# Performance work log

Hardware: AMD Instinct MI355X
Metric: run time of the kernel (lower is better)

The kernel has to match this reference:

```python
import jax, jax.numpy as jnp
import numpy as np

N = 100000          # num_nodes
E = 1600000         # num_edges (avg degree 16)
FEAT = 16           # z-embedding dim
IN_DIM = FEAT + 4   # + 4 physics scalars
HID = 128           # hidden_dim
NUM_LAYERS = 2
NUM_REL = 3
NUM_TYPES = 4
LN_EPS = 1e-5


def setup_inputs() -> dict:
    key = jax.random.key(0)
    ks = jax.random.split(key, 20)
    s = 0.05
    return {
        "z": jax.random.randint(ks[0], (N,), 0, 100),
        "sd": jax.random.normal(ks[1], (N, 1), jnp.float32),
        "df": jax.random.normal(ks[2], (N, 1), jnp.float32),
        "cond": jax.random.normal(ks[3], (N, 1), jnp.float32),
        "mult": jax.random.normal(ks[4], (N, 1), jnp.float32),
        "node_type": jax.random.randint(ks[5], (N,), 0, NUM_TYPES),
        "edge_index": jax.random.randint(ks[6], (2, E), 0, N),
        "edge_type": jax.random.randint(ks[7], (E,), 0, NUM_REL),
        # parameters
        "z_embed": jax.random.normal(ks[8], (100, FEAT), jnp.float32) * s,
        "enc_W1": jax.random.normal(ks[9], (NUM_TYPES, IN_DIM, HID), jnp.float32) * s,
        "enc_b1": jnp.zeros((NUM_TYPES, HID), jnp.float32),
        "enc_W2": jax.random.normal(ks[10], (NUM_TYPES, HID, HID), jnp.float32) * s,
        "enc_b2": jnp.zeros((NUM_TYPES, HID), jnp.float32),
        "lin_W": jax.random.normal(ks[11], (NUM_LAYERS, HID, HID), jnp.float32) * s,
        "lin_b": jnp.zeros((NUM_LAYERS, HID), jnp.float32),
        "rel_W": jax.random.normal(ks[12], (NUM_LAYERS, NUM_REL, HID, HID), jnp.float32) * s,
        "ln_g": jnp.ones((NUM_LAYERS, HID), jnp.float32),
        "ln_b": jnp.zeros((NUM_LAYERS, HID), jnp.float32),
        "reg_W": jax.random.normal(ks[13], (HID, 1), jnp.float32) * s,
        "reg_b": jnp.zeros((1,), jnp.float32),
    }


def reference(z, sd, df, cond, mult, node_type, edge_index, edge_type,
              z_embed, enc_W1, enc_b1, enc_W2, enc_b2,
              lin_W, lin_b, rel_W, ln_g, ln_b, reg_W, reg_b):
    # FeatureBuilder: [z embedding | 4 physics scalars] -> [N, IN_DIM]
    raw = jnp.concatenate([z_embed[z], sd, df, cond, mult], axis=1)
    n = raw.shape[0]

    # TypeSpecificEncoder: per-node-type 2-layer MLP, selected by node_type
    x = jnp.zeros((n, enc_W2.shape[-1]), raw.dtype)
    for t in range(enc_W1.shape[0]):
        h = jax.nn.relu(raw @ enc_W1[t] + enc_b1[t]) @ enc_W2[t] + enc_b2[t]
        x = jnp.where((node_type == t)[:, None], h, x)

    src, dst = edge_index[0], edge_index[1]
    # degree over ALL edges (as in the torch code), clamped to >= 1
    deg = jax.ops.segment_sum(jnp.ones(src.shape[0], x.dtype), dst, num_segments=n)
    deg = jnp.clip(deg, 1.0)[:, None]

    # stacked MultiRelationGNNLayer: gather -> per-relation matmul -> scatter-add
    for l in range(lin_W.shape[0]):
        xs = x[src]                               # [E, HID] gather
        msg = jnp.zeros_like(xs)
        for r in range(rel_W.shape[1]):
            mask_r = (edge_type == r)[:, None].astype(x.dtype)
            msg = msg + (xs @ rel_W[l, r]) * mask_r
        agg = jax.ops.segment_sum(msg, dst, num_segments=n) / deg
        h = x @ lin_W[l] + lin_b[l] + agg
        # LayerNorm
        mu = jnp.mean(h, axis=-1, keepdims=True)
        var = jnp.mean((h - mu) ** 2, axis=-1, keepdims=True)
        x = (h - mu) / jnp.sqrt(var + LN_EPS) * ln_g[l] + ln_b[l]

    pooled = jnp.mean(x, axis=0)                  # [HID]
    return pooled @ reg_W + reg_b                 # [1]
```

## Files before the change

### kernel.cpp

```cpp
#include <hip/hip_runtime.h>

#define NN 100000
#define NE 1600000
#define HD 128
#define IND 20
#define LNEPS 1e-5f
#define NLIST2 400000
#define NBKT 3125
#define PASSA_B 256
#define EDGES_PER_B 6250
#define FILL_B 256
#define WCAT_B 512
#define WCATE_B 256
#define W1P_B 128
#define FILLN_B 400
#define ENC_B 12500
#define ASTRIDE 260
#define SORT_CAP 4096
#define PAD_PER_BKT 672
#define NEP (NE + NBKT * PAD_PER_BKT)
#define H1S 136
#define AES 72

typedef unsigned int uint32;
typedef unsigned short ushort16;
typedef __attribute__((ext_vector_type(8))) short bf16x8;
typedef __attribute__((ext_vector_type(4))) float f32x4;
typedef __attribute__((ext_vector_type(2))) float f32x2;

__device__ __forceinline__ ushort16 f2bf(float f) {
    uint32 u = __float_as_uint(f);
    u += 0x7fffu + ((u >> 16) & 1u);
    return (ushort16)(u >> 16);
}
__device__ __forceinline__ float bf2f1(ushort16 h) {
    return __uint_as_float(((uint32)h) << 16);
}
__device__ __forceinline__ uint32 pack2bf(float2 v) {
    return (uint32)f2bf(v.x) | ((uint32)f2bf(v.y) << 16);
}


__global__ __launch_bounds__(256) void k_hist(const int* __restrict__ ei,
                                              const int* __restrict__ et,
                                              int* __restrict__ H,
                                              ushort16* __restrict__ key16,
                                              unsigned* __restrict__ hdr32,
                                              const float* __restrict__ W2,
                                              ushort16* __restrict__ Weh,
                                              ushort16* __restrict__ Wel,
                                              const float* __restrict__ W1,
                                              ushort16* __restrict__ W1e,
                                              const int* __restrict__ nt,
                                              int* misc, unsigned* nodelist,
                                              uint32* x0, uint32* x1) {
    __shared__ int hist[NBKT];
    __shared__ int cnt4[4][4];
    __shared__ int base4[4];
    int bid = blockIdx.x, tid = threadIdx.x;

    if (bid >= PASSA_B + WCATE_B + W1P_B) {
        int rb = bid - PASSA_B - WCATE_B - W1P_B;
        int lane = tid & 63;
        int w = tid >> 6;
        if (rb == 0 && tid < 32) {
            x0[(size_t)NN * 32 + tid] = 0;
            x1[(size_t)NN * 32 + tid] = 0;
        }
        int i = rb * 256 + tid;
        int t = (i < NN) ? nt[i] : -1;
        unsigned long long lt = ((unsigned long long)1 << lane) - 1;
        int pre[4], wc[4];
#pragma unroll
        for (int tt = 0; tt < 4; tt++) {
            unsigned long long m = __ballot(t == tt);
            pre[tt] = (int)__popcll(m & lt);
            wc[tt] = (int)__popcll(m);
        }
        if (lane == 0) {
            cnt4[w][0] = wc[0]; cnt4[w][1] = wc[1];
            cnt4[w][2] = wc[2]; cnt4[w][3] = wc[3];
        }
        __syncthreads();
        if (tid < 4) {
            int tot = cnt4[0][tid] + cnt4[1][tid] + cnt4[2][tid] + cnt4[3][tid];
            base4[tid] = tot ? atomicAdd(&misc[8 + tid], tot) : 0;
        }
        __syncthreads();
        if (t >= 0) {
            int off = base4[t] + pre[t];
#pragma unroll
            for (int wp = 0; wp < 3; wp++) if (wp < w) off += cnt4[wp][t];
            nodelist[t * NN + off] = (unsigned)i | ((unsigned)t << 17);
        }
        return;
    }
    if (bid >= PASSA_B + WCATE_B) {
        int idx = (bid - PASSA_B - WCATE_B) * 256 + tid;
        int jj = idx & 7;
        int lane = (idx >> 3) & 63;
        int ntile = (idx >> 9) & 7;
        int kstep = (idx >> 12) & 1;
        int t = (idx >> 13) & 3;
        int ke = kstep * 32 + ((lane >> 4) * 8) + jj;
        int n = ntile * 16 + (lane & 15);
        float w = 0.f;
        int sel = 0;
        if (ke < 60) {
            int k0 = ke / 3;
            sel = ke - 3 * k0;
            w = W1[((size_t)t * IND + k0) * HD + n];
        }
        ushort16 hi = f2bf(w);
        W1e[idx] = (sel == 2) ? f2bf(w - bf2f1(hi)) : hi;
        return;
    }
    if (bid >= PASSA_B) {
        int idx = (bid - PASSA_B) * 256 + tid;
        int jj = idx & 7;
        int lane = (idx >> 3) & 63;
        int ntile = (idx >> 9) & 7;
        int kt = (idx >> 12) & 3;
        int t = (idx >> 14) & 3;
        int k = kt * 32 + ((lane >> 4) * 8) + jj;
        int n = ntile * 16 + (lane & 15);
        float v = W2[((size_t)t * HD + k) * HD + n];
        ushort16 hi = f2bf(v);
        Weh[idx] = hi;
        Wel[idx] = f2bf(v - bf2f1(hi));
        return;
    }

    for (int k = tid; k < NBKT; k += 256) hist[k] = 0;
    __syncthreads();
    int e0 = bid * EDGES_PER_B, e1 = e0 + EDGES_PER_B;
    for (int e = e0 + tid; e < e1; e += 256) {
        int d = ei[NE + e];
        int s = ei[e];
        int r = et[e];
        int bkt = d >> 5;
        key16[e] = (ushort16)bkt;
        hdr32[e] = (unsigned)s | ((unsigned)r << 17) | ((unsigned)(d & 31) << 19);
        atomicAdd(&hist[bkt], 1);
    }
    __syncthreads();
    for (int k = tid; k < NBKT; k += 256) H[bid * NBKT + k] = hist[k];
}


__global__ __launch_bounds__(256) void k_s1(int* __restrict__ H, int* __restrict__ btot) {
    int bkt = blockIdx.x * 256 + threadIdx.x;
    if (bkt >= NBKT) return;
    int run = 0;
    for (int jm = 0; jm < PASSA_B; jm += 8) {
        int t0 = H[(jm + 0) * NBKT + bkt];
        int t1 = H[(jm + 1) * NBKT + bkt];
        int t2 = H[(jm + 2) * NBKT + bkt];
        int t3 = H[(jm + 3) * NBKT + bkt];
        int t4 = H[(jm + 4) * NBKT + bkt];
        int t5 = H[(jm + 5) * NBKT + bkt];
        int t6 = H[(jm + 6) * NBKT + bkt];
        int t7 = H[(jm + 7) * NBKT + bkt];
        H[(jm + 0) * NBKT + bkt] = run; run += t0;
        H[(jm + 1) * NBKT + bkt] = run; run += t1;
        H[(jm + 2) * NBKT + bkt] = run; run += t2;
        H[(jm + 3) * NBKT + bkt] = run; run += t3;
        H[(jm + 4) * NBKT + bkt] = run; run += t4;
        H[(jm + 5) * NBKT + bkt] = run; run += t5;
        H[(jm + 6) * NBKT + bkt] = run; run += t6;
        H[(jm + 7) * NBKT + bkt] = run; run += t7;
    }
    btot[bkt] = run;
}

__global__ __launch_bounds__(1024) void k_s2(const int* __restrict__ btot,
                                             int* __restrict__ boff) {
    __shared__ int s[1024];
    int t = threadIdx.x;
    int v4[4];
    int sum = 0;
#pragma unroll
    for (int i = 0; i < 4; i++) {
        int idx = t * 4 + i;
        v4[i] = (idx < NBKT) ? btot[idx] : 0;
        sum += v4[i];
    }
    s[t] = sum;
    __syncthreads();
    for (int o = 1; o < 1024; o <<= 1) {
        int tv = (t >= o) ? s[t - o] : 0;
        __syncthreads();
        s[t] += tv;
        __syncthreads();
    }
    int run = s[t] - sum;
#pragma unroll
    for (int i = 0; i < 4; i++) {
        int idx = t * 4 + i;
        if (idx < NBKT) boff[idx] = run;
        run += v4[i];
    }
    if (t == 1023) boff[NBKT] = NE;
}


__global__ __launch_bounds__(256) void k_fill2(
        const ushort16* __restrict__ key16, const unsigned* __restrict__ hdr32,
        const int* __restrict__ H, const int* __restrict__ boff,
        unsigned* __restrict__ packed,
        const unsigned* __restrict__ nodelist, const int* __restrict__ z,
        const float* __restrict__ sd, const float* __restrict__ df,
        const float* __restrict__ cond, const float* __restrict__ mult,
        const float* __restrict__ z_embed,
        const ushort16* __restrict__ W1e, const float* __restrict__ b1,
        const float* __restrict__ b2,
        unsigned char* __restrict__ xout,
        const float* __restrict__ rel_W, const float* __restrict__ lin_W,
        ushort16* __restrict__ Wbh, ushort16* __restrict__ Wbl,
        const ushort16* __restrict__ Weh, const ushort16* __restrict__ Wel) {
    __shared__ __attribute__((aligned(16))) char smem[13440];
    int bid = blockIdx.x;
    int tid = threadIdx.x;

    if (bid < FILL_B) {
        int* cur = (int*)smem;
        for (int k = tid; k < NBKT; k += 256)
            cur[k] = boff[k] + H[bid * NBKT + k];
        __syncthreads();
        int e0 = bid * EDGES_PER_B, e1 = e0 + EDGES_PER_B;
        for (int e = e0 + tid; e < e1; e += 256) {
            int kb = (int)key16[e];
            int p = atomicAdd(&cur[kb], 1);
            packed[p] = hdr32[e];
        }
        return;
    }
    int j = bid - FILL_B;
    if (j < WCAT_B) {
        int idx = j * 256 + tid;
        int jj = idx & 7;
        int lane = (idx >> 3) & 63;
        int ntile = (idx >> 9) & 7;
        int kt = (idx >> 12) & 15;
        int l = (idx >> 16) & 1;
        int k = kt * 32 + ((lane >> 4) * 8) + jj;
        int n = ntile * 16 + (lane & 15);
        float v;
        if (k < 384) v = rel_W[((l * 3 + (k >> 7)) * HD + (k & 127)) * HD + n];
        else         v = lin_W[(l * HD + (k - 384)) * HD + n];
        ushort16 hi = f2bf(v);
        Wbh[idx] = hi;
        Wbl[idx] = f2bf(v - bf2f1(hi));
        return;
    }
    j -= WCAT_B;
    if (j >= ENC_B) return;

    ushort16* Ae  = (ushort16*)smem;
    ushort16* h1b = (ushort16*)(smem + 4608);
    unsigned* ent = (unsigned*)(smem + 4608 + 8704);

    int base = j * 32;
    if (tid < 32) ent[tid] = nodelist[base + tid];
    if (tid >= 64 && tid < 128) {
        int r = (tid - 64) >> 1, c = 30 + (tid & 1);
        ((uint32*)Ae)[r * 36 + c] = 0;
    }
    __syncthreads();
    if (ent[0] == 0xFFFFFFFFu) return;
    int type = (int)(ent[0] >> 17);

    for (int idx = tid; idx < 32 * 20; idx += 256) {
        int nl = idx / 20, f = idx - nl * 20;
        unsigned e = ent[nl];
        float v = 0.f;
        if (e != 0xFFFFFFFFu) {
            int node = (int)(e & 0x1FFFF);
            if (f < 16)      v = z_embed[z[node] * 16 + f];
            else if (f == 16) v = sd[node];
            else if (f == 17) v = df[node];
            else if (f == 18) v = cond[node];
            else              v = mult[node];
        }
        ushort16 hi = f2bf(v);
        ushort16 lo = f2bf(v - bf2f1(hi));
        ushort16* ap = Ae + nl * AES + 3 * f;
        ap[0] = hi; ap[1] = lo; ap[2] = hi;
    }
    __syncthreads();

    int lane = tid & 63, wv = tid >> 6;
    int nt0 = 2 * wv, nt1 = 2 * wv + 1;
    int mrow0 = lane & 15, mrow1 = 16 + (lane & 15);
    int koff = (lane >> 4) * 8;

    {
        f32x4 e00 = {0.f, 0.f, 0.f, 0.f}, e01 = e00, e10 = e00, e11 = e00;
        const bf16x8* w1p = (const bf16x8*)(W1e + (size_t)type * 8192);
#pragma unroll
        for (int ks = 0; ks < 2; ks++) {
            bf16x8 af0 = *(const bf16x8*)&Ae[mrow0 * AES + ks * 32 + koff];
            bf16x8 af1 = *(const bf16x8*)&Ae[mrow1 * AES + ks * 32 + koff];
            bf16x8 bf0 = w1p[(ks * 8 + nt0) * 64 + lane];
            bf16x8 bf1 = w1p[(ks * 8 + nt1) * 64 + lane];
            e00 = __builtin_amdgcn_mfma_f32_16x16x32_bf16(af0, bf0, e00, 0, 0, 0);
            e01 = __builtin_amdgcn_mfma_f32_16x16x32_bf16(af0, bf1, e01, 0, 0, 0);
            e10 = __builtin_amdgcn_mfma_f32_16x16x32_bf16(af1, bf0, e10, 0, 0, 0);
            e11 = __builtin_amdgcn_mfma_f32_16x16x32_bf16(af1, bf1, e11, 0, 0, 0);
        }
        int c0 = nt0 * 16 + (lane & 15), c1 = nt1 * 16 + (lane & 15);
        float bb0 = b1[type * HD + c0], bb1 = b1[type * HD + c1];
        int rb2 = (lane >> 4) * 4;
#pragma unroll
        for (int r = 0; r < 4; r++) {
            h1b[(rb2 + r) * H1S + c0]      = f2bf(fmaxf(e00[r] + bb0, 0.f));
            h1b[(rb2 + r) * H1S + c1]      = f2bf(fmaxf(e01[r] + bb1, 0.f));
            h1b[(16 + rb2 + r) * H1S + c0] = f2bf(fmaxf(e10[r] + bb0, 0.f));
            h1b[(16 + rb2 + r) * H1S + c1] = f2bf(fmaxf(e11[r] + bb1, 0.f));
        }
    }
    __syncthreads();

    f32x4 a00 = {0.f, 0.f, 0.f, 0.f}, a01 = a00, a10 = a00, a11 = a00;
    const bf16x8* weh = (const bf16x8*)(Weh + (size_t)type * 16384);
    const bf16x8* wel = (const bf16x8*)(Wel + (size_t)type * 16384);
    const ushort16* h1p = h1b;
#pragma unroll
    for (int kt = 0; kt < 4; kt++) {
        bf16x8 af0 = *(const bf16x8*)&h1p[mrow0 * H1S + kt * 32 + koff];
        bf16x8 af1 = *(const bf16x8*)&h1p[mrow1 * H1S + kt * 32 + koff];
        bf16x8 bh0 = weh[(kt * 8 + nt0) * 64 + lane];
        bf16x8 bh1 = weh[(kt * 8 + nt1) * 64 + lane];
        bf16x8 bl0 = wel[(kt * 8 + nt0) * 64 + lane];
        bf16x8 bl1 = wel[(kt * 8 + nt1) * 64 + lane];
        a00 = __builtin_amdgcn_mfma_f32_16x16x32_bf16(af0, bh0, a00, 0, 0, 0);
        a01 = __builtin_amdgcn_mfma_f32_16x16x32_bf16(af0, bh1, a01, 0, 0, 0);
        a10 = __builtin_amdgcn_mfma_f32_16x16x32_bf16(af1, bh0, a10, 0, 0, 0);
        a11 = __builtin_amdgcn_mfma_f32_16x16x32_bf16(af1, bh1, a11, 0, 0, 0);
        a00 = __builtin_amdgcn_mfma_f32_16x16x32_bf16(af0, bl0, a00, 0, 0, 0);
        a01 = __builtin_amdgcn_mfma_f32_16x16x32_bf16(af0, bl1, a01, 0, 0, 0);
        a10 = __builtin_amdgcn_mfma_f32_16x16x32_bf16(af1, bl0, a10, 0, 0, 0);
        a11 = __builtin_amdgcn_mfma_f32_16x16x32_bf16(af1, bl1, a11, 0, 0, 0);
    }
    int c0 = nt0 * 16 + (lane & 15), c1 = nt1 * 16 + (lane & 15);
    float b20 = b2[type * HD + c0], b21 = b2[type * HD + c1];
    int rb = (lane >> 4) * 4;
#pragma unroll
    for (int r = 0; r < 4; r++) {
        int r0 = rb + r, r1 = 16 + rb + r;
        unsigned e0v = ent[r0], e1v = ent[r1];
        if (e0v != 0xFFFFFFFFu) {
            int node = (int)(e0v & 0x1FFFF);
            int p0 = __builtin_amdgcn_cvt_pk_fp8_f32(a00[r] + b20, a00[r] + b20, 0, false);
            int p1 = __builtin_amdgcn_cvt_pk_fp8_f32(a01[r] + b21, a01[r] + b21, 0, false);
            xout[(size_t)node * HD + c0] = (unsigned char)(p0 & 0xff);
            xout[(size_t)node * HD + c1] = (unsigned char)(p1 & 0xff);
        }
        if (e1v != 0xFFFFFFFFu) {
            int node = (int)(e1v & 0x1FFFF);
            int p0 = __builtin_amdgcn_cvt_pk_fp8_f32(a10[r] + b20, a10[r] + b20, 0, false);
            int p1 = __builtin_amdgcn_cvt_pk_fp8_f32(a11[r] + b21, a11[r] + b21, 0, false);
            xout[(size_t)node * HD + c0] = (unsigned char)(p0 & 0xff);
            xout[(size_t)node * HD + c1] = (unsigned char)(p1 & 0xff);
        }
    }
}


__global__ __launch_bounds__(256) void k_sort2(const unsigned* __restrict__ packed,
                                               const int* __restrict__ boff,
                                               unsigned* __restrict__ packed2,
                                               int* __restrict__ off,
                                               int* __restrict__ degarr) {
    __shared__ unsigned ebuf[SORT_CAP];
    __shared__ int hs[96];
    __shared__ int cur[96];
    __shared__ int segp[97];
    __shared__ int scn[128];
    int b = blockIdx.x;
    int tid = threadIdx.x;
    int base = boff[b];
    int tot = boff[b + 1] - base;
    if (tot > SORT_CAP) tot = SORT_CAP;
    int pb = base + PAD_PER_BKT * b;

    if (tid < 96) hs[tid] = 0;
    for (int e = tid; e < tot; e += 256) ebuf[e] = packed[base + e];
    __syncthreads();
    for (int e = tid; e < tot; e += 256) {
        unsigned h = ebuf[e];
        int key = (int)(h >> 19) * 3 + (int)((h >> 17) & 3);
        atomicAdd(&hs[key], 1);
    }
    __syncthreads();
    int padv = (tid < 96) ? ((hs[tid] + 7) & ~7) : 0;
    if (tid < 128) scn[tid] = padv;
    __syncthreads();
#pragma unroll
    for (int o = 1; o < 128; o <<= 1) {
        int tv = (tid < 128 && tid >= o) ? scn[tid - o] : 0;
        __syncthreads();
        if (tid < 128) scn[tid] += tv;
        __syncthreads();
    }
    if (tid < 96) segp[tid] = scn[tid] - padv;
    if (tid == 95) segp[96] = scn[95];
    __syncthreads();
    if (tid < 96) {
        cur[tid] = segp[tid];
        off[((b * 32 + tid / 3) << 2) + (tid % 3)] = pb + segp[tid];
    }
    if (tid >= 96 && tid < 128) {
        int n = tid - 96;
        off[((b * 32 + n) << 2) + 3] = pb + segp[3 * n + 3];
        degarr[b * 32 + n] = hs[3 * n] + hs[3 * n + 1] + hs[3 * n + 2];
    }
    __syncthreads();
    for (int e = tid; e < tot; e += 256) {
        unsigned h = ebuf[e];
        int key = (int)(h >> 19) * 3 + (int)((h >> 17) & 3);
        int p = atomicAdd(&cur[key], 1);
        packed2[pb + p] = h & 0x1FFFF;
    }
    __syncthreads();
    if (tid < 96) {
        int e0 = segp[tid] + hs[tid];
        int e1 = segp[tid + 1];
        for (int q = e0; q < e1; q++) packed2[pb + q] = NN;
    }
}


#define LOADU8(U, Q)                                                          \
    U##0 = x[(int)Q##0 * 64 + lane]; U##1 = x[(int)Q##1 * 64 + lane];         \
    U##2 = x[(int)Q##2 * 64 + lane]; U##3 = x[(int)Q##3 * 64 + lane];         \
    U##4 = x[(int)Q##4 * 64 + lane]; U##5 = x[(int)Q##5 * 64 + lane];         \
    U##6 = x[(int)Q##6 * 64 + lane]; U##7 = x[(int)Q##7 * 64 + lane];

#define LOADQ8(Q, E)                                                          \
    Q##0 = packed[(E)];     Q##1 = packed[(E) + 1];                           \
    Q##2 = packed[(E) + 2]; Q##3 = packed[(E) + 3];                           \
    Q##4 = packed[(E) + 4]; Q##5 = packed[(E) + 5];                           \
    Q##6 = packed[(E) + 6]; Q##7 = packed[(E) + 7];

#define SUM8(S, U) {                                                          \
    f32x2 v0 = __builtin_amdgcn_cvt_pk_f32_fp8(U##0, false);                  \
    f32x2 v1 = __builtin_amdgcn_cvt_pk_f32_fp8(U##1, false);                  \
    f32x2 v2 = __builtin_amdgcn_cvt_pk_f32_fp8(U##2, false);                  \
    f32x2 v3 = __builtin_amdgcn_cvt_pk_f32_fp8(U##3, false);                  \
    f32x2 v4 = __builtin_amdgcn_cvt_pk_f32_fp8(U##4, false);                  \
    f32x2 v5 = __builtin_amdgcn_cvt_pk_f32_fp8(U##5, false);                  \
    f32x2 v6 = __builtin_amdgcn_cvt_pk_f32_fp8(U##6, false);                  \
    f32x2 v7 = __builtin_amdgcn_cvt_pk_f32_fp8(U##7, false);                  \
    S = ((v0 + v1) + (v2 + v3)) + ((v4 + v5) + (v6 + v7)); }

__global__ __launch_bounds__(512, 6) void k_fused(
        const ushort16* __restrict__ x,
        const unsigned* __restrict__ packed,
        const int* __restrict__ off, const int* __restrict__ degarr,
        const ushort16* __restrict__ Wbh, const ushort16* __restrict__ Wbl,
        const float* __restrict__ lb, const float* __restrict__ g,
        const float* __restrict__ bta, unsigned char* __restrict__ xout,
        const float* __restrict__ regW, float* __restrict__ partials) {
    __shared__ uint32 Alds[32 * ASTRIDE];
    __shared__ float stat[32][2];
    __shared__ float red[8];
    int tid = threadIdx.x;
    int lane = tid & 63;
    int wv = tid >> 6;
    int nb = blockIdx.x * 32;

    int bv = off[((nb + wv * 4) << 2) + lane];
    int dgv = degarr[nb + wv * 4 + (lane & 3)];

#pragma unroll
    for (int p = 0; p < 2; p++) {
        int nodeA = nb + wv * 4 + 2 * p;
        int nodeB = nodeA + 1;
        int bA0 = __builtin_amdgcn_readlane(bv, 8 * p + 0);
        int bA1 = __builtin_amdgcn_readlane(bv, 8 * p + 1);
        int bA2 = __builtin_amdgcn_readlane(bv, 8 * p + 2);
        int bA3 = __builtin_amdgcn_readlane(bv, 8 * p + 3);
        int bB0 = __builtin_amdgcn_readlane(bv, 8 * p + 4);
        int bB1 = __builtin_amdgcn_readlane(bv, 8 * p + 5);
        int bB2 = __builtin_amdgcn_readlane(bv, 8 * p + 6);
        int bB3 = __builtin_amdgcn_readlane(bv, 8 * p + 7);
        int dgA = __builtin_amdgcn_readlane(dgv, 2 * p);
        int dgB = __builtin_amdgcn_readlane(dgv, 2 * p + 1);
        float idA = 1.0f / (float)(dgA > 0 ? dgA : 1);
        float idB = 1.0f / (float)(dgB > 0 ? dgB : 1);
        int usA = x[nodeA * 64 + lane];
        int usB = x[nodeB * 64 + lane];
        f32x2 aA0 = {0.f, 0.f}, aA1 = aA0, aA2 = aA0;
        f32x2 aB0 = aA0, aB1 = aA0, aB2 = aA0;
        int eA = bA0, eB = bB0;
        unsigned qA0, qA1, qA2, qA3, qA4, qA5, qA6, qA7;
        unsigned qB0, qB1, qB2, qB3, qB4, qB5, qB6, qB7;
        if (eA < bA3) { LOADQ8(qA, eA) }
        if (eB < bB3) { LOADQ8(qB, eB) }
        while (true) {
            bool dA = eA < bA3, dB = eB < bB3;
            if (!dA && !dB) break;
            int uA0, uA1, uA2, uA3, uA4, uA5, uA6, uA7;
            int uB0, uB1, uB2, uB3, uB4, uB5, uB6, uB7;
            if (dA) { LOADU8(uA, qA) }
            if (dB) { LOADU8(uB, qB) }
            if (dA) { LOADQ8(qA, eA + 8) }
            if (dB) { LOADQ8(qB, eB + 8) }
            if (dA) {
                f32x2 s; SUM8(s, uA)
                if (eA < bA1)      aA0 += s;
                else if (eA < bA2) aA1 += s;
                else               aA2 += s;
                eA += 8;
            }
            if (dB) {
                f32x2 s; SUM8(s, uB)
                if (eB < bB1)      aB0 += s;
                else if (eB < bB2) aB1 += s;
                else               aB2 += s;
                eB += 8;
            }
        }
        uint32* arA = Alds + (wv * 4 + 2 * p) * ASTRIDE;
        uint32* arB = arA + ASTRIDE;
        f32x2 vsA = __builtin_amdgcn_cvt_pk_f32_fp8(usA, false);
        f32x2 vsB = __builtin_amdgcn_cvt_pk_f32_fp8(usB, false);
        arA[lane]       = pack2bf(make_float2(aA0.x * idA, aA0.y * idA));
        arA[64 + lane]  = pack2bf(make_float2(aA1.x * idA, aA1.y * idA));
        arA[128 + lane] = pack2bf(make_float2(aA2.x * idA, aA2.y * idA));
        arA[192 + lane] = pack2bf(make_float2(vsA.x, vsA.y));
        arB[lane]       = pack2bf(make_float2(aB0.x * idB, aB0.y * idB));
        arB[64 + lane]  = pack2bf(make_float2(aB1.x * idB, aB1.y * idB));
        arB[128 + lane] = pack2bf(make_float2(aB2.x * idB, aB2.y * idB));
        arB[192 + lane] = pack2bf(make_float2(vsB.x, vsB.y));
    }
    __syncthreads();

    f32x4 acc00 = {0.f, 0.f, 0.f, 0.f}, acc10 = acc00;
    int mrow0 = (lane & 15);
    int mrow1 = 16 + (lane & 15);
    int q4 = (lane >> 4) * 4;
    const bf16x8* wbh = (const bf16x8*)Wbh;
    const bf16x8* wbl = (const bf16x8*)Wbl;

#pragma unroll 4
    for (int kt = 0; kt < 16; kt++) {
        bf16x8 af0 = *(const bf16x8*)&Alds[mrow0 * ASTRIDE + kt * 16 + q4];
        bf16x8 af1 = *(const bf16x8*)&Alds[mrow1 * ASTRIDE + kt * 16 + q4];
        bf16x8 bh0 = wbh[(kt * 8 + wv) * 64 + lane];
        bf16x8 bl0 = wbl[(kt * 8 + wv) * 64 + lane];
        acc00 = __builtin_amdgcn_mfma_f32_16x16x32_bf16(af0, bh0, acc00, 0, 0, 0);
        acc10 = __builtin_amdgcn_mfma_f32_16x16x32_bf16(af1, bh0, acc10, 0, 0, 0);
        acc00 = __builtin_amdgcn_mfma_f32_16x16x32_bf16(af0, bl0, acc00, 0, 0, 0);
        acc10 = __builtin_amdgcn_mfma_f32_16x16x32_bf16(af1, bl0, acc10, 0, 0, 0);
    }
    __syncthreads();

    float* hlds = (float*)Alds;
    int n0 = wv * 16 + (lane & 15);
    float bj0 = lb[n0];
    int rbase = (lane >> 4) * 4;
#pragma unroll
    for (int r = 0; r < 4; r++) {
        hlds[(rbase + r) * 132 + n0]      = acc00[r] + bj0;
        hlds[(16 + rbase + r) * 132 + n0] = acc10[r] + bj0;
    }
    __syncthreads();

    {
        int node = tid >> 4, l16 = tid & 15;
        float s = 0.f, ss = 0.f;
#pragma unroll
        for (int i = 0; i < 8; i++) {
            float v = hlds[node * 132 + l16 + 16 * i];
            s += v; ss += v * v;
        }
        for (int d = 8; d >= 1; d >>= 1) {
            s += __shfl_down(s, d, 16);
            ss += __shfl_down(ss, d, 16);
        }
        if (l16 == 0) {
            float mu = s * (1.f / 128.f);
            float var = ss * (1.f / 128.f) - mu * mu;
            stat[node][0] = mu;
            stat[node][1] = rsqrtf(var + LNEPS);
        }
    }
    __syncthreads();

    {
        int node = tid >> 4, q16 = tid & 15;
        float mu = stat[node][0], rs = stat[node][1];
        const float* hr = hlds + node * 132 + q16 * 8;
        float vv[8];
#pragma unroll
        for (int k = 0; k < 8; k++) {
            int f = q16 * 8 + k;
            vv[k] = (hr[k] - mu) * rs * g[f] + bta[f];
        }
        if (regW == nullptr) {
            int w[2];
#pragma unroll
            for (int p = 0; p < 2; p++) {
                int pk = __builtin_amdgcn_cvt_pk_fp8_f32(vv[p * 4 + 0], vv[p * 4 + 1], 0, false);
                pk = __builtin_amdgcn_cvt_pk_fp8_f32(vv[p * 4 + 2], vv[p * 4 + 3], pk, true);
                w[p] = pk;
            }
            *(int2*)(xout + (size_t)(nb + node) * 128 + q16 * 8) = make_int2(w[0], w[1]);
        } else {
            float s = 0.f;
#pragma unroll
            for (int k = 0; k < 8; k++) s += vv[k] * regW[q16 * 8 + k];
            for (int d = 32; d >= 1; d >>= 1) s += __shfl_down(s, d);
            if (lane == 0) red[wv] = s;
            __syncthreads();
            if (tid == 0) {
                partials[blockIdx.x] = red[0] + red[1] + red[2] + red[3] +
                                       red[4] + red[5] + red[6] + red[7];
            }
        }
    }
}


__global__ __launch_bounds__(1024) void k_red(const float* __restrict__ partials,
                                              const float* __restrict__ reg_b,
                                              float* __restrict__ out) {
    __shared__ float s[16];
    int tid = threadIdx.x;
    float v = 0.f;
    for (int i = tid; i < NBKT; i += 1024) v += partials[i];
    for (int d = 32; d >= 1; d >>= 1) v += __shfl_down(v, d);
    if ((tid & 63) == 0) s[tid >> 6] = v;
    __syncthreads();
    if (tid == 0) {
        float t = 0.f;
#pragma unroll
        for (int i = 0; i < 16; i++) t += s[i];
        out[0] = t * (1.0f / (float)NN) + reg_b[0];
    }
}


extern "C" void kernel_launch(void* const* d_in, const int* in_sizes, int n_in,
                              void* d_out, int out_size, void* d_ws, size_t ws_size,
                              hipStream_t stream) {
    const int*   z       = (const int*)d_in[0];
    const float* sd      = (const float*)d_in[1];
    const float* df      = (const float*)d_in[2];
    const float* cond    = (const float*)d_in[3];
    const float* mult    = (const float*)d_in[4];
    const int*   nt      = (const int*)d_in[5];
    const int*   ei      = (const int*)d_in[6];
    const int*   et      = (const int*)d_in[7];
    const float* z_embed = (const float*)d_in[8];
    const float* enc_W1  = (const float*)d_in[9];
    const float* enc_b1  = (const float*)d_in[10];
    const float* enc_W2  = (const float*)d_in[11];
    const float* enc_b2  = (const float*)d_in[12];
    const float* lin_W   = (const float*)d_in[13];
    const float* lin_b   = (const float*)d_in[14];
    const float* rel_W   = (const float*)d_in[15];
    const float* ln_g    = (const float*)d_in[16];
    const float* ln_b    = (const float*)d_in[17];
    const float* reg_W   = (const float*)d_in[18];
    const float* reg_b   = (const float*)d_in[19];
    float* out = (float*)d_out;

    char* p = (char*)d_ws;
    int* H          = (int*)p;      p += (size_t)PASSA_B * NBKT * 4;
    int* btot       = (int*)p;      p += (size_t)4096 * 4;
    int* boff       = (int*)p;      p += (size_t)4096 * 4;
    int* misc       = (int*)p;      p += 16 * 4;
    float* partials = (float*)p;    p += (size_t)4096 * 4;
    int* off        = (int*)p;      p += (size_t)400384 * 4;
    int* degarr     = (int*)p;      p += (size_t)100096 * 4;
    ushort16* key16 = (ushort16*)p; p += (size_t)NE * 2;
    unsigned* hdr32 = (unsigned*)p; p += (size_t)NE * 4;
    unsigned* packed   = (unsigned*)p; p += (size_t)NE * 4;
    unsigned* packed2  = (unsigned*)p; p += (size_t)(NEP + 16) * 4;
    unsigned* nodelist = (unsigned*)p; p += (size_t)NLIST2 * 4;
    ushort16* Wbh   = (ushort16*)p; p += (size_t)2 * 512 * 128 * 2;
    ushort16* Wbl   = (ushort16*)p; p += (size_t)2 * 512 * 128 * 2;
    ushort16* Weh   = (ushort16*)p; p += (size_t)65536 * 2;
    ushort16* Wel   = (ushort16*)p; p += (size_t)65536 * 2;
    ushort16* W1e   = (ushort16*)p; p += (size_t)32768 * 2;
    unsigned char* x0 = (unsigned char*)p; p += (size_t)(NN + 1) * HD;
    unsigned char* x1 = (unsigned char*)p; p += (size_t)(NN + 1) * HD;

    hipMemsetAsync(misc, 0, 64, stream);
    hipMemsetAsync(nodelist, 0xFF, (size_t)NLIST2 * 4, stream);

    k_hist<<<PASSA_B + WCATE_B + W1P_B + FILLN_B, 256, 0, stream>>>(
        ei, et, H, key16, hdr32, enc_W2, Weh, Wel, enc_W1, W1e,
        nt, misc, nodelist, (uint32*)x0, (uint32*)x1);
    k_s1<<<13, 256, 0, stream>>>(H, btot);
    k_s2<<<1, 1024, 0, stream>>>(btot, boff);
    k_fill2<<<FILL_B + WCAT_B + ENC_B, 256, 0, stream>>>(
        key16, hdr32, H, boff, packed,
        nodelist, z, sd, df, cond, mult, z_embed,
        W1e, enc_b1, enc_b2, x0,
        rel_W, lin_W, Wbh, Wbl, Weh, Wel);
    k_sort2<<<NBKT, 256, 0, stream>>>(packed, boff, packed2, off, degarr);

    k_fused<<<NBKT, 512, 0, stream>>>((const ushort16*)x0, packed2, off, degarr,
                                      Wbh, Wbl,
                                      lin_b, ln_g, ln_b,
                                      x1, nullptr, partials);
    k_fused<<<NBKT, 512, 0, stream>>>((const ushort16*)x1, packed2, off, degarr,
                                      Wbh + (size_t)512 * 128, Wbl + (size_t)512 * 128,
                                      lin_b + HD, ln_g + HD, ln_b + HD,
                                      x0, reg_W, partials);
    k_red<<<1, 1024, 0, stream>>>(partials, reg_b, out);
}
```

Measured before the change: 340.4 us.

## Split per-bucket histogram column scan into chunked two-pass scan

Replaces the single-kernel column-wise exclusive scan over the 256 per-block histograms with a two-pass scheme. The first kernel sums 8 chunks of 32 rows per bucket, and the second computes chunk bases and writes the exclusive offsets. This exposes 8x more threads and shortens each thread's serial dependent load chain. The cost is an extra kernel launch, a small scratch buffer, and re-reading H.

```diff
diff --git a/kernel.cpp b/kernel.cpp
--- a/kernel.cpp
+++ b/kernel.cpp
@@ -148,29 +148,37 @@
 }
 
 
-__global__ __launch_bounds__(256) void k_s1(int* __restrict__ H, int* __restrict__ btot) {
-    int bkt = blockIdx.x * 256 + threadIdx.x;
-    if (bkt >= NBKT) return;
-    int run = 0;
-    for (int jm = 0; jm < PASSA_B; jm += 8) {
-        int t0 = H[(jm + 0) * NBKT + bkt];
-        int t1 = H[(jm + 1) * NBKT + bkt];
-        int t2 = H[(jm + 2) * NBKT + bkt];
-        int t3 = H[(jm + 3) * NBKT + bkt];
-        int t4 = H[(jm + 4) * NBKT + bkt];
-        int t5 = H[(jm + 5) * NBKT + bkt];
-        int t6 = H[(jm + 6) * NBKT + bkt];
-        int t7 = H[(jm + 7) * NBKT + bkt];
-        H[(jm + 0) * NBKT + bkt] = run; run += t0;
-        H[(jm + 1) * NBKT + bkt] = run; run += t1;
-        H[(jm + 2) * NBKT + bkt] = run; run += t2;
-        H[(jm + 3) * NBKT + bkt] = run; run += t3;
-        H[(jm + 4) * NBKT + bkt] = run; run += t4;
-        H[(jm + 5) * NBKT + bkt] = run; run += t5;
-        H[(jm + 6) * NBKT + bkt] = run; run += t6;
-        H[(jm + 7) * NBKT + bkt] = run; run += t7;
-    }
-    btot[bkt] = run;
+__global__ __launch_bounds__(256) void k_s1a(const int* __restrict__ H,
+                                             int* __restrict__ csum) {
+    int idx = blockIdx.x * 256 + threadIdx.x;
+    if (idx >= 8 * NBKT) return;
+    int c = idx / NBKT;
+    int bkt = idx - c * NBKT;
+    const int* hp = H + (size_t)(c * 32) * NBKT + bkt;
+    int s = 0;
+#pragma unroll 8
+    for (int r = 0; r < 32; r++) s += hp[(size_t)r * NBKT];
+    csum[idx] = s;
+}
+
+__global__ __launch_bounds__(256) void k_s1b(int* __restrict__ H,
+                                             const int* __restrict__ csum,
+                                             int* __restrict__ btot) {
+    int idx = blockIdx.x * 256 + threadIdx.x;
+    if (idx >= 8 * NBKT) return;
+    int c = idx / NBKT;
+    int bkt = idx - c * NBKT;
+    int base = 0;
+    for (int j = 0; j < c; j++) base += csum[j * NBKT + bkt];
+    if (c == 7) btot[bkt] = base + csum[7 * NBKT + bkt];
+    int* hp = H + (size_t)(c * 32) * NBKT + bkt;
+    int run = base;
+#pragma unroll 8
+    for (int r = 0; r < 32; r++) {
+        int t = hp[(size_t)r * NBKT];
+        hp[(size_t)r * NBKT] = run;
+        run += t;
+    }
 }
 
 __global__ __launch_bounds__(1024) void k_s2(const int* __restrict__ btot,
@@ -672,6 +680,7 @@
     int* H          = (int*)p;      p += (size_t)PASSA_B * NBKT * 4;
     int* btot       = (int*)p;      p += (size_t)4096 * 4;
     int* boff       = (int*)p;      p += (size_t)4096 * 4;
+    int* csum       = (int*)p;      p += (size_t)8 * NBKT * 4;
     int* misc       = (int*)p;      p += 16 * 4;
     float* partials = (float*)p;    p += (size_t)4096 * 4;
     int* off        = (int*)p;      p += (size_t)400384 * 4;
@@ -695,7 +704,8 @@
     k_hist<<<PASSA_B + WCATE_B + W1P_B + FILLN_B, 256, 0, stream>>>(
         ei, et, H, key16, hdr32, enc_W2, Weh, Wel, enc_W1, W1e,
         nt, misc, nodelist, (uint32*)x0, (uint32*)x1);
-    k_s1<<<13, 256, 0, stream>>>(H, btot);
+    k_s1a<<<(8 * NBKT + 255) / 256, 256, 0, stream>>>(H, csum);
+    k_s1b<<<(8 * NBKT + 255) / 256, 256, 0, stream>>>(H, csum, btot);
     k_s2<<<1, 1024, 0, stream>>>(btot, boff);
     k_fill2<<<FILL_B + WCAT_B + ENC_B, 256, 0, stream>>>(
         key16, hdr32, H, boff, packed,
```

Result: slower. 347.5 us (+2.1%).
